# Performance work log

Measured on AMD Instinct MI355X. Metric: run time of the kernel, lower is better.

## Reference

```python
import jax, jax.numpy as jnp
import numpy as np

B = 4096
IN_DIM = 256
OUT_DIM = 256
COND_DIM = 128
HID = 512
HYPER_OUT = IN_DIM * OUT_DIM  # 65536


def setup_inputs() -> dict:
    key = jax.random.key(0)
    ks = jax.random.split(key, 8)

    def xavier(k, shape):
        fan_in, fan_out = shape[0], shape[1]
        std = np.sqrt(2.0 / (fan_in + fan_out))
        return jax.random.normal(k, shape, dtype=jnp.float32) * std

    return {
        "input_h": jax.random.normal(ks[0], (B, IN_DIM), dtype=jnp.float32),
        "condition_z": jax.random.normal(ks[1], (B, COND_DIM), dtype=jnp.float32),
        # hypernet: Linear(COND_DIM, HID) -> ReLU -> Linear(HID, HYPER_OUT)
        "W1": xavier(ks[2], (COND_DIM, HID)),
        "b1": jnp.zeros((HID,), dtype=jnp.float32),
        "W2": xavier(ks[3], (HID, HYPER_OUT)),
        "b2": jnp.zeros((HYPER_OUT,), dtype=jnp.float32),
        # static bias (use_bias=True, generate_bias=False)
        "bias": jnp.zeros((1, OUT_DIM), dtype=jnp.float32),
    }


def reference(input_h, condition_z, W1, b1, W2, b2, bias):
    # HyperNet MLP generates per-sample weight matrix
    hyp = jax.nn.relu(condition_z @ W1 + b1)          # [B, HID]
    weight_S = hyp @ W2 + b2                          # [B, IN*OUT]  (1 GB intermediate)
    weight_S = weight_S.reshape(-1, IN_DIM, OUT_DIM)  # [B, IN, OUT]
    # batched matmul: [B,1,IN] x [B,IN,OUT] -> [B,OUT]
    out = jnp.einsum("bi,bio->bo", input_h, weight_S)
    return out + bias
```

## Files before the change

kernel.cpp:

```cpp
#include <hip/hip_runtime.h>
#include <hip/hip_bf16.h>
#include <stdint.h>


typedef __bf16 bf16x8 __attribute__((ext_vector_type(8)));
typedef float  f32x4  __attribute__((ext_vector_type(4)));

#define KTILES     2052
#define TILE_BYTES 32768
#define HB_OFF     (9u*1024u*1024u)
#define BP_OFF     (12u*1024u*1024u)

__global__ void k_init_out(const float* __restrict__ bias, float* __restrict__ out) {
    int idx = blockIdx.x * 256 + threadIdx.x;
    out[idx] = bias[idx & 255];
}

__global__ void k_hcast(const float* __restrict__ h, uint16_t* __restrict__ hb) {
    int i = (blockIdx.x * 256 + threadIdx.x) * 8;
    f32x4 a = *(const f32x4*)(h + i);
    f32x4 b = *(const f32x4*)(h + i + 4);
    bf16x8 v;
    v[0] = (__bf16)a[0]; v[1] = (__bf16)a[1]; v[2] = (__bf16)a[2]; v[3] = (__bf16)a[3];
    v[4] = (__bf16)b[0]; v[5] = (__bf16)b[1]; v[6] = (__bf16)b[2]; v[7] = (__bf16)b[3];
    *(bf16x8*)(hb + i) = v;
}

__global__ void k_hypT(const float* __restrict__ z, const float* __restrict__ W1,
                       const float* __restrict__ b1, float* __restrict__ hypT) {
    int blk = blockIdx.x;
    int t   = threadIdx.x;
    if (blk == 128) {
#pragma unroll
        for (int r = 0; r < 8; ++r) hypT[(size_t)512*4096 + r*512 + t] = 1.0f;
        return;
    }
    __shared__ float zs[32][128];
    int b0 = blk * 32;
#pragma unroll
    for (int u = 0; u < 8; ++u) {
        int idx = u * 512 + t;
        zs[idx >> 7][idx & 127] = z[b0 * 128 + idx];
    }
    __syncthreads();
    float acc[32];
    float bk = b1[t];
#pragma unroll
    for (int b = 0; b < 32; ++b) acc[b] = bk;
    for (int c = 0; c < 128; ++c) {
        float w = W1[c * 512 + t];
#pragma unroll
        for (int b = 0; b < 32; ++b) acc[b] = fmaf(zs[b][c], w, acc[b]);
    }
    float* dst = hypT + (size_t)t * 4096 + b0;
#pragma unroll
    for (int v = 0; v < 8; ++v) {
        f32x4 o;
#pragma unroll
        for (int q = 0; q < 4; ++q) {
            float a = acc[v * 4 + q];
            o[q] = a > 0.f ? a : 0.f;
        }
        *(f32x4*)(dst + v * 4) = o;
    }
}

__global__ void k_pack(const float* __restrict__ W2, const float* __restrict__ b2,
                       uint16_t* __restrict__ Bp) {
    __shared__ char tile[TILE_BYTES];
    int t   = blockIdx.x;
    int tid = threadIdx.x;
    long row0 = (long)t * 64;
    const float* src = (t < 2048) ? (W2 + row0 * 256) : (b2 + (row0 - 131072) * 256);
#pragma unroll
    for (int u = 0; u < 16; ++u) {
        int f = (u * 256 + tid) * 4;
        f32x4 v = *(const f32x4*)(src + f);
        int kk = f >> 8;
        int o0 = f & 255;
#pragma unroll
        for (int j = 0; j < 4; ++j) {
            int o = o0 + j;
            int addr = (o * 128 + kk * 2) ^ ((o & 7) << 4);
            *(__bf16*)(tile + addr) = (__bf16)v[j];
        }
    }
    __syncthreads();
    char* dst = (char*)Bp + (size_t)t * TILE_BYTES;
#pragma unroll
    for (int v = 0; v < 8; ++v) {
        int off = (v * 256 + tid) * 16;
        *(f32x4*)(dst + off) = *(const f32x4*)(tile + off);
    }
}

__global__ __launch_bounds__(512, 2) void k_gemm(
        const uint16_t* __restrict__ hb, const float* __restrict__ hypT,
        const uint16_t* __restrict__ Bp, float* __restrict__ out) {
    __shared__ char smem[131072];

    const int tid  = threadIdx.x;
    const int lane = tid & 63;
    const int wid  = tid >> 6;
    const int l15  = lane & 15, lg = lane >> 4;

    const int bid = blockIdx.x;
    const int s   = bid & 7;
    const int mt  = bid >> 3;
    const int k0  = s * 64;
    const int row_base = mt * 128;
    const int NT  = (s == 7) ? 260 : 256;
    const int colw = wid * 32;

    float* shyp = (float*)(smem + 98304);

#pragma unroll
    for (int u = 0; u < 4; ++u) {
        int f  = (u * 512 + tid) * 4;
        int kk = f >> 7;
        int r  = f & 127;
        *(f32x4*)(shyp + kk * 128 + r) =
            *(const f32x4*)(hypT + (size_t)(k0 + kk) * 4096 + row_base + r);
    }

    auto tile_of = [&](int idx) {
        return (idx < 256) ? ((k0 + (idx & 63)) * 4 + (idx >> 6)) : (2048 + idx - 256);
    };
    auto stage = [&](int bufoff, int t) {
        const char* gsrc = (const char*)Bp + (size_t)t * TILE_BYTES + wid * 4096 + lane * 16;
        char* ldst = smem + bufoff + wid * 4096;
#pragma unroll
        for (int q = 0; q < 4; ++q)
            __builtin_amdgcn_global_load_lds(
                (const __attribute__((address_space(1))) void*)(gsrc + q * 1024),
                (__attribute__((address_space(3))) void*)(ldst + q * 1024), 16, 0, 0);
    };

    stage(0,     tile_of(0));
    stage(32768, tile_of(1));
    asm volatile("s_waitcnt vmcnt(4) lgkmcnt(0)" ::: "memory");
    __builtin_amdgcn_s_barrier();

    f32x4 acc[8][2];
#pragma unroll
    for (int i = 0; i < 8; ++i)
#pragma unroll
        for (int j = 0; j < 2; ++j)
#pragma unroll
            for (int q = 0; q < 4; ++q) acc[i][j][q] = 0.0f;

    const f32x4 fzero = {0.f, 0.f, 0.f, 0.f};
    int boff_read = 0, boff_next = 32768, boff_stage = 65536;

    for (int G = 0; G < 8; ++G) {
        if (G >= 4 && s != 7) break;
        const int niter = (G < 4) ? 64 : 1;

        bf16x8 af[8][2];
#pragma unroll
        for (int mf = 0; mf < 8; ++mf)
#pragma unroll
            for (int ks = 0; ks < 2; ++ks)
                af[mf][ks] = *(const bf16x8*)(hb + (size_t)(row_base + mf * 16 + l15) * 256
                                              + (G & 3) * 64 + ks * 32 + lg * 8);

        for (int jj = 0; jj < niter; ++jj) {
            const int idx = (G < 4) ? G * 64 + jj : 256 + (G - 4);
            const bool do_stage = (idx + 2 < NT);
            if (do_stage) stage(boff_stage, tile_of(idx + 2));

            const char* sB = smem + boff_read;
            bf16x8 b0[2], b1[2];
#pragma unroll
            for (int nf = 0; nf < 2; ++nf) {
                int col = colw + nf * 16 + l15;
                int swz = (col & 7) << 4;
                b0[nf] = *(const bf16x8*)(sB + ((col * 128 + lg * 16) ^ swz));
                b1[nf] = *(const bf16x8*)(sB + ((col * 128 + 64 + lg * 16) ^ swz));
            }
            f32x4 scv[8];
            if (idx < 256) {
#pragma unroll
                for (int mf = 0; mf < 8; ++mf)
                    scv[mf] = *(const f32x4*)(shyp + jj * 128 + mf * 16 + lg * 4);
            } else {
#pragma unroll
                for (int mf = 0; mf < 8; ++mf) scv[mf] = {1.f, 1.f, 1.f, 1.f};
            }

            asm volatile("" ::: "memory");
            __builtin_amdgcn_s_barrier();
            asm volatile("" ::: "memory");

            __builtin_amdgcn_s_setprio(1);
#pragma unroll
            for (int mf = 0; mf < 8; ++mf)
#pragma unroll
                for (int nf = 0; nf < 2; ++nf) {
                    f32x4 p = __builtin_amdgcn_mfma_f32_16x16x32_bf16(af[mf][0], b0[nf], fzero, 0, 0, 0);
                    p = __builtin_amdgcn_mfma_f32_16x16x32_bf16(af[mf][1], b1[nf], p, 0, 0, 0);
#pragma unroll
                    for (int q = 0; q < 4; ++q)
                        acc[mf][nf][q] = fmaf(scv[mf][q], p[q], acc[mf][nf][q]);
                }
            __builtin_amdgcn_s_setprio(0);

            if (do_stage) asm volatile("s_waitcnt vmcnt(4)" ::: "memory");
            else          asm volatile("s_waitcnt vmcnt(0)" ::: "memory");
            __builtin_amdgcn_s_barrier();

            int tmp = boff_read; boff_read = boff_next; boff_next = boff_stage; boff_stage = tmp;
        }
    }

#pragma unroll
    for (int mf = 0; mf < 8; ++mf)
#pragma unroll
        for (int nf = 0; nf < 2; ++nf) {
            int col = colw + nf * 16 + l15;
#pragma unroll
            for (int q = 0; q < 4; ++q) {
                int row = row_base + mf * 16 + lg * 4 + q;
                atomicAdd(&out[row * 256 + col], acc[mf][nf][q]);
            }
        }
}

extern "C" void kernel_launch(void* const* d_in, const int* in_sizes, int n_in,
                              void* d_out, int out_size, void* d_ws, size_t ws_size,
                              hipStream_t stream) {
    const float* h    = (const float*)d_in[0];
    const float* z    = (const float*)d_in[1];
    const float* W1   = (const float*)d_in[2];
    const float* b1   = (const float*)d_in[3];
    const float* W2   = (const float*)d_in[4];
    const float* b2   = (const float*)d_in[5];
    const float* bias = (const float*)d_in[6];
    float* out = (float*)d_out;

    float*    hypT = (float*)d_ws;
    uint16_t* hb   = (uint16_t*)((char*)d_ws + HB_OFF);
    uint16_t* Bp   = (uint16_t*)((char*)d_ws + BP_OFF);

    k_pack    <<<KTILES, 256, 0, stream>>>(W2, b2, Bp);
    k_hypT    <<<129,    512, 0, stream>>>(z, W1, b1, hypT);
    k_hcast   <<<512,    256, 0, stream>>>(h, hb);
    k_init_out<<<4096,   256, 0, stream>>>(bias, out);
    k_gemm    <<<256,    512, 0, stream>>>(hb, hypT, Bp, out);
}
```

Baseline: 376.2 us.

## Process two B tiles per iteration with four-slot LDS ring, one barrier per pair

The GEMM main loop now consumes two 32KB B tiles per iteration from a four-slot LDS ring (160KB of LDS). It issues two stages ahead and drops the mid-iteration barrier, so barriers are halved. The bias tiles are handled in a separate tail loop. The cost is one block per CU instead of two, since launch bounds and LDS use grow, and each iteration waits with vmcnt(0), so prefetch overlap is shallower.

New measurement: 925.9 us. 2.46x slower.

```diff
diff --git a/kernel.cpp b/kernel.cpp
--- a/kernel.cpp
+++ b/kernel.cpp
@@ -94,10 +94,10 @@
     }
 }
 
-__global__ __launch_bounds__(512, 2) void k_gemm(
+__global__ __launch_bounds__(512, 1) void k_gemm(
         const uint16_t* __restrict__ hb, const float* __restrict__ hypT,
         const uint16_t* __restrict__ Bp, float* __restrict__ out) {
-    __shared__ char smem[131072];
+    __shared__ char smem[163840];
 
     const int tid  = threadIdx.x;
     const int lane = tid & 63;
@@ -112,7 +112,7 @@
     const int NT  = (s == 7) ? 260 : 256;
     const int colw = wid * 32;
 
-    float* shyp = (float*)(smem + 98304);
+    float* shyp = (float*)(smem + 131072);
 
 #pragma unroll
     for (int u = 0; u < 4; ++u) {
@@ -126,9 +126,9 @@
     auto tile_of = [&](int idx) {
         return (idx < 256) ? ((k0 + (idx & 63)) * 4 + (idx >> 6)) : (2048 + idx - 256);
     };
-    auto stage = [&](int bufoff, int t) {
+    auto stage = [&](int slot, int t) {
         const char* gsrc = (const char*)Bp + (size_t)t * TILE_BYTES + wid * 4096 + lane * 16;
-        char* ldst = smem + bufoff + wid * 4096;
+        char* ldst = smem + (slot << 15) + wid * 4096;
 #pragma unroll
         for (int q = 0; q < 4; ++q)
             __builtin_amdgcn_global_load_lds(
@@ -136,9 +136,9 @@
                 (__attribute__((address_space(3))) void*)(ldst + q * 1024), 16, 0, 0);
     };
 
-    stage(0,     tile_of(0));
-    stage(32768, tile_of(1));
-    asm volatile("s_waitcnt vmcnt(4) lgkmcnt(0)" ::: "memory");
+    stage(0, tile_of(0));
+    stage(1, tile_of(1));
+    asm volatile("s_waitcnt vmcnt(0) lgkmcnt(0)" ::: "memory");
     __builtin_amdgcn_s_barrier();
 
     f32x4 acc[8][2];
@@ -150,66 +150,98 @@
             for (int q = 0; q < 4; ++q) acc[i][j][q] = 0.0f;
 
     const f32x4 fzero = {0.f, 0.f, 0.f, 0.f};
-    int boff_read = 0, boff_next = 32768, boff_stage = 65536;
-
-    for (int G = 0; G < 8; ++G) {
-        if (G >= 4 && s != 7) break;
-        const int niter = (G < 4) ? 64 : 1;
-
+
+    for (int G = 0; G < 4; ++G) {
         bf16x8 af[8][2];
 #pragma unroll
         for (int mf = 0; mf < 8; ++mf)
 #pragma unroll
             for (int ks = 0; ks < 2; ++ks)
                 af[mf][ks] = *(const bf16x8*)(hb + (size_t)(row_base + mf * 16 + l15) * 256
-                                              + (G & 3) * 64 + ks * 32 + lg * 8);
-
-        for (int jj = 0; jj < niter; ++jj) {
-            const int idx = (G < 4) ? G * 64 + jj : 256 + (G - 4);
-            const bool do_stage = (idx + 2 < NT);
-            if (do_stage) stage(boff_stage, tile_of(idx + 2));
-
-            const char* sB = smem + boff_read;
-            bf16x8 b0[2], b1[2];
+                                              + G * 64 + ks * 32 + lg * 8);
+
+        for (int jj = 0; jj < 32; ++jj) {
+            const int idx0 = G * 64 + jj * 2;
+            if (idx0 + 2 < NT) stage((idx0 + 2) & 3, tile_of(idx0 + 2));
+            if (idx0 + 3 < NT) stage((idx0 + 3) & 3, tile_of(idx0 + 3));
+
+            const char* sB0 = smem + ((idx0 & 3) << 15);
+            const char* sB1 = smem + (((idx0 + 1) & 3) << 15);
+            bf16x8 b00[2], b01[2], b10[2], b11[2];
 #pragma unroll
             for (int nf = 0; nf < 2; ++nf) {
                 int col = colw + nf * 16 + l15;
                 int swz = (col & 7) << 4;
-                b0[nf] = *(const bf16x8*)(sB + ((col * 128 + lg * 16) ^ swz));
-                b1[nf] = *(const bf16x8*)(sB + ((col * 128 + 64 + lg * 16) ^ swz));
-            }
-            f32x4 scv[8];
-            if (idx < 256) {
-#pragma unroll
-                for (int mf = 0; mf < 8; ++mf)
-                    scv[mf] = *(const f32x4*)(shyp + jj * 128 + mf * 16 + lg * 4);
-            } else {
-#pragma unroll
-                for (int mf = 0; mf < 8; ++mf) scv[mf] = {1.f, 1.f, 1.f, 1.f};
-            }
-
-            asm volatile("" ::: "memory");
-            __builtin_amdgcn_s_barrier();
-            asm volatile("" ::: "memory");
+                int o0  = (col * 128 + lg * 16) ^ swz;
+                int o1  = (col * 128 + 64 + lg * 16) ^ swz;
+                b00[nf] = *(const bf16x8*)(sB0 + o0);
+                b01[nf] = *(const bf16x8*)(sB0 + o1);
+                b10[nf] = *(const bf16x8*)(sB1 + o0);
+                b11[nf] = *(const bf16x8*)(sB1 + o1);
+            }
+            f32x4 scv0[8], scv1[8];
+#pragma unroll
+            for (int mf = 0; mf < 8; ++mf) {
+                scv0[mf] = *(const f32x4*)(shyp + (jj * 2) * 128 + mf * 16 + lg * 4);
+                scv1[mf] = *(const f32x4*)(shyp + (jj * 2 + 1) * 128 + mf * 16 + lg * 4);
+            }
 
             __builtin_amdgcn_s_setprio(1);
 #pragma unroll
             for (int mf = 0; mf < 8; ++mf)
 #pragma unroll
                 for (int nf = 0; nf < 2; ++nf) {
-                    f32x4 p = __builtin_amdgcn_mfma_f32_16x16x32_bf16(af[mf][0], b0[nf], fzero, 0, 0, 0);
-                    p = __builtin_amdgcn_mfma_f32_16x16x32_bf16(af[mf][1], b1[nf], p, 0, 0, 0);
+                    f32x4 p = __builtin_amdgcn_mfma_f32_16x16x32_bf16(af[mf][0], b00[nf], fzero, 0, 0, 0);
+                    p = __builtin_amdgcn_mfma_f32_16x16x32_bf16(af[mf][1], b01[nf], p, 0, 0, 0);
 #pragma unroll
                     for (int q = 0; q < 4; ++q)
-                        acc[mf][nf][q] = fmaf(scv[mf][q], p[q], acc[mf][nf][q]);
+                        acc[mf][nf][q] = fmaf(scv0[mf][q], p[q], acc[mf][nf][q]);
+                }
+#pragma unroll
+            for (int mf = 0; mf < 8; ++mf)
+#pragma unroll
+                for (int nf = 0; nf < 2; ++nf) {
+                    f32x4 p = __builtin_amdgcn_mfma_f32_16x16x32_bf16(af[mf][0], b10[nf], fzero, 0, 0, 0);
+                    p = __builtin_amdgcn_mfma_f32_16x16x32_bf16(af[mf][1], b11[nf], p, 0, 0, 0);
+#pragma unroll
+                    for (int q = 0; q < 4; ++q)
+                        acc[mf][nf][q] = fmaf(scv1[mf][q], p[q], acc[mf][nf][q]);
                 }
             __builtin_amdgcn_s_setprio(0);
 
-            if (do_stage) asm volatile("s_waitcnt vmcnt(4)" ::: "memory");
-            else          asm volatile("s_waitcnt vmcnt(0)" ::: "memory");
+            asm volatile("s_waitcnt vmcnt(0)" ::: "memory");
             __builtin_amdgcn_s_barrier();
-
-            int tmp = boff_read; boff_read = boff_next; boff_next = boff_stage; boff_stage = tmp;
+        }
+    }
+
+    if (s == 7) {
+        for (int g = 0; g < 4; ++g) {
+            int idx = 256 + g;
+            if (idx + 2 < 260) stage((idx + 2) & 3, tile_of(idx + 2));
+            bf16x8 af[8][2];
+#pragma unroll
+            for (int mf = 0; mf < 8; ++mf)
+#pragma unroll
+                for (int ks = 0; ks < 2; ++ks)
+                    af[mf][ks] = *(const bf16x8*)(hb + (size_t)(row_base + mf * 16 + l15) * 256
+                                                  + g * 64 + ks * 32 + lg * 8);
+            const char* sB = smem + ((idx & 3) << 15);
+#pragma unroll
+            for (int nf = 0; nf < 2; ++nf) {
+                int col = colw + nf * 16 + l15;
+                int swz = (col & 7) << 4;
+                bf16x8 u0 = *(const bf16x8*)(sB + ((col * 128 + lg * 16) ^ swz));
+                bf16x8 u1 = *(const bf16x8*)(sB + ((col * 128 + 64 + lg * 16) ^ swz));
+#pragma unroll
+                for (int mf = 0; mf < 8; ++mf) {
+                    f32x4 p = __builtin_amdgcn_mfma_f32_16x16x32_bf16(af[mf][0], u0, fzero, 0, 0, 0);
+                    p = __builtin_amdgcn_mfma_f32_16x16x32_bf16(af[mf][1], u1, p, 0, 0, 0);
+#pragma unroll
+                    for (int q = 0; q < 4; ++q) acc[mf][nf][q] += p[q];
+                }
+            }
+            asm volatile("s_waitcnt vmcnt(0)" ::: "memory");
+            __builtin_amdgcn_s_barrier();
         }
     }
 
```
